# Kernel optimization log

Measured on AMD Instinct MI355X. Metric: run time of the kernel, lower is better.

## Reference

```python
import jax, jax.numpy as jnp
import numpy as np

B, H, W = 4, 240, 1216
PROP = 6


def conv2d(x, w, b, pad=0, groups=1):
    out = jax.lax.conv_general_dilated(
        x, w, (1, 1), ((pad, pad), (pad, pad)),
        dimension_numbers=('NCHW', 'OIHW', 'NCHW'),
        feature_group_count=groups)
    return out + b[None, :, None, None]


def affinity(g, ww, wb, ow, ob):
    # g: [B,8,H,W] -> offset [B,18,H,W] (y,x pairs per kernel pt), weight [B,9,H,W]
    wgt = jax.nn.sigmoid(conv2d(g, ww, wb, pad=1))
    wgt = wgt / (jnp.sum(wgt, axis=1, keepdims=True) + 1e-8)
    off = conv2d(g, ow, ob, pad=1)                      # [B,16,H,W]
    off = off.reshape(B, 8, 2, H, W)
    zero = jnp.zeros((B, 1, 2, H, W), off.dtype)
    off = jnp.concatenate([off[:, :4], zero, off[:, 4:]], axis=1)  # zero offset at reference (center) point, idx 4
    return off.reshape(B, 18, H, W), wgt


def bilinear_gather(img, py, px):
    # img [B,H,W]; py/px [B,9,H,W]; zero padding outside the image
    y0 = jnp.floor(py); x0 = jnp.floor(px)
    wy = py - y0; wx = px - x0
    y0i = y0.astype(jnp.int32); x0i = x0.astype(jnp.int32)
    flat = img.reshape(B, -1)
    out = jnp.zeros_like(py)
    for dy, dx, wgt in ((0, 0, (1 - wy) * (1 - wx)), (0, 1, (1 - wy) * wx),
                        (1, 0, wy * (1 - wx)), (1, 1, wy * wx)):
        yy = y0i + dy; xx = x0i + dx
        valid = (yy >= 0) & (yy < H) & (xx >= 0) & (xx < W)
        idx = (jnp.clip(yy, 0, H - 1) * W + jnp.clip(xx, 0, W - 1)).reshape(B, -1)
        v = jnp.take_along_axis(flat, idx, axis=1).reshape(B, 9, H, W)
        out = out + wgt * jnp.where(valid, v, 0.0)
    return out


def mdconv(feat, offset, mask, w3, b3):
    # Modulated deformable conv (DCNv2), 3x3, stride 1, pad 1, dil 1,
    # groups = C = 1, weight w3 [1,1,3,3] (ones), bias b3 [1] (zero).
    off = offset.reshape(B, 9, 2, H, W)
    ky = jnp.repeat(jnp.arange(3), 3).astype(feat.dtype)   # kernel row for k = i*3+j
    kx = jnp.tile(jnp.arange(3), 3).astype(feat.dtype)
    gy = jnp.arange(H, dtype=feat.dtype)
    gx = jnp.arange(W, dtype=feat.dtype)
    py = gy[None, None, :, None] - 1.0 + ky[None, :, None, None] + off[:, :, 0]
    px = gx[None, None, None, :] - 1.0 + kx[None, :, None, None] + off[:, :, 1]
    samp = bilinear_gather(feat[:, 0], py, px)             # [B,9,H,W]
    out = jnp.einsum('bkhw,k->bhw', mask * samp, w3.reshape(9)) + b3[0]
    return out[:, None]


def _forward(feat_init, guidance, attn, aff_w_w, aff_w_b, aff_o_w, aff_o_b,
             w3, b3, proj_w, bn_g, bn_b, c0_w, c0_b, cs_w, cs_b,
             c1_w, c1_b, c2_w, c2_b, csq_w, csq_b, cv_w, cv_b):
    feats = []
    feat = feat_init
    for k in range(PROP):  # fixed, small structural loop (distinct params per step)
        g = guidance[:, 8 * k:8 * (k + 1)]
        off, wgt = affinity(g, aff_w_w[k], aff_w_b[k], aff_o_w[k], aff_o_b[k])
        feat = mdconv(feat, off, wgt, w3, b3)
        feats.append(feat)
    y = jnp.concatenate(feats[3:6], axis=1)                # [B,3,H,W]
    # proj: 1x1 conv (no bias) -> BatchNorm (training-mode stats) -> LeakyReLU(0.2)
    sf = conv2d(y, proj_w, jnp.zeros((6,), y.dtype), pad=0)
    mu = jnp.mean(sf, axis=(0, 2, 3), keepdims=True)
    var = jnp.var(sf, axis=(0, 2, 3), keepdims=True)
    sf = (sf - mu) * jax.lax.rsqrt(var + 1e-5)
    sf = sf * bn_g[None, :, None, None] + bn_b[None, :, None, None]
    sf = jnp.where(sf > 0, sf, 0.2 * sf)
    x = jnp.concatenate([attn, sf], axis=1)                # [B,22,H,W]
    # CrossAttn(dim=22)
    a1 = conv2d(x, c0_w, c0_b, pad=0, groups=22)           # depthwise 1x1
    a2 = conv2d(a1, cs_w, cs_b, pad=1, groups=22)          # depthwise 3x3
    a1 = conv2d(a1, c1_w, c1_b)                            # 22 -> 11
    a2 = conv2d(a2, c2_w, c2_b)                            # 22 -> 11
    ac = jnp.concatenate([a1, a2], axis=1)                 # [B,22,H,W]
    agg = jnp.concatenate([jnp.mean(ac, axis=1, keepdims=True),
                           jnp.max(ac, axis=1, keepdims=True)], axis=1)
    sig = jax.nn.sigmoid(conv2d(agg, csq_w, csq_b, pad=1))
    a = a1 * sig[:, 0:1] + a2 * sig[:, 1:2]
    a = conv2d(a, cv_w, cv_b)                              # [B,3,H,W]
    return jnp.sum(y * a, axis=1, keepdims=True)           # [B,1,H,W]


def setup_inputs() -> dict:
    key = jax.random.key(0)
    ks = jax.random.split(key, 16)
    n = lambda k, s, sc=1.0: sc * jax.random.normal(k, s, dtype=jnp.float32)
    return {
        'feat_init': n(ks[0], (B, 1, H, W)),
        'guidance': n(ks[1], (B, 48, H, W)),
        'attn': n(ks[2], (B, 16, H, W)),
        'feat_fix': n(ks[3], (B, 1, H, W)),
        'aff_w_w': n(ks[4], (PROP, 9, 8, 3, 3), 0.1),
        'aff_w_b': jnp.zeros((PROP, 9), jnp.float32),
        'aff_o_w': n(ks[5], (PROP, 16, 8, 3, 3), 0.05),
        'aff_o_b': jnp.zeros((PROP, 16), jnp.float32),
        'w3': jnp.ones((1, 1, 3, 3), jnp.float32),
        'b3': jnp.zeros((1,), jnp.float32),
        'proj_w': n(ks[6], (6, 3, 1, 1), 0.3),
        'bn_g': jnp.ones((6,), jnp.float32),
        'bn_b': jnp.zeros((6,), jnp.float32),
        'c0_w': n(ks[7], (22, 1, 1, 1), 0.3),
        'c0_b': jnp.zeros((22,), jnp.float32),
        'cs_w': n(ks[8], (22, 1, 3, 3), 0.2),
        'cs_b': jnp.zeros((22,), jnp.float32),
        'c1_w': n(ks[9], (11, 22, 1, 1), 0.2),
        'c1_b': jnp.zeros((11,), jnp.float32),
        'c2_w': n(ks[10], (11, 22, 1, 1), 0.2),
        'c2_b': jnp.zeros((11,), jnp.float32),
        'csq_w': n(ks[11], (2, 2, 3, 3), 0.2),
        'csq_b': jnp.zeros((2,), jnp.float32),
        'cv_w': n(ks[12], (3, 11, 1, 1), 0.2),
        'cv_b': jnp.zeros((3,), jnp.float32),
    }


def reference(feat_init, guidance, attn, feat_fix, aff_w_w, aff_w_b, aff_o_w, aff_o_b,
              w3, b3, proj_w, bn_g, bn_b, c0_w, c0_b, cs_w, cs_b,
              c1_w, c1_b, c2_w, c2_b, csq_w, csq_b, cv_w, cv_b):
    # mask_fix = sign(feat_fix) is computed in the original but never used.
    _ = jnp.sign(feat_fix)
    return _forward(feat_init, guidance, attn, aff_w_w, aff_w_b, aff_o_w, aff_o_b,
                    w3, b3, proj_w, bn_g, bn_b, c0_w, c0_b, cs_w, cs_b,
                    c1_w, c1_b, c2_w, c2_b, csq_w, csq_b, cv_w, cv_b)
```

## Files before the change

### kernel.cpp

```cpp
#include <hip/hip_runtime.h>
#include <hip/hip_bf16.h>
#include <math.h>

#define HH 240
#define WW 1216
#define BATCH 4
#define PROP 6
constexpr int HW = HH * WW;
constexpr int NPIX = BATCH * HW;
constexpr int NPART = 1024;

typedef short short8 __attribute__((ext_vector_type(8)));
typedef float floatx4 __attribute__((ext_vector_type(4)));

__device__ __forceinline__ unsigned short f2bf(float f) {
    unsigned int u = __float_as_uint(f);
    unsigned int r = (u + 0x7FFFu + ((u >> 16) & 1u)) >> 16;
    return (unsigned short)r;
}
__device__ __forceinline__ float bf2f(unsigned short h) {
    return __uint_as_float(((unsigned int)h) << 16);
}

constexpr int CT_STRIDE = 25;
constexpr int SMEM_BYTES = 23360;

__global__ __launch_bounds__(256, 4) void prop_kernel(
    const float* __restrict__ featPrev,
    const float* __restrict__ gbase,
    const float* __restrict__ aw,
    const float* __restrict__ ab,
    const float* __restrict__ ow,
    const float* __restrict__ ob,
    const float* __restrict__ w3,
    const float* __restrict__ b3,
    float* __restrict__ featNext)
{
    __shared__ __attribute__((aligned(16))) unsigned char smem[SMEM_BYTES];
    unsigned short* gs16 = (unsigned short*)smem;
    float*    wst    = (float*)(smem + 10560);
    uint32_t* offtab = (uint32_t*)(smem + 22848);
    unsigned short* ctb = (unsigned short*)(smem + 10560);

    const int tid = threadIdx.x;
    const int x0 = blockIdx.x * 64;
    const int y0t = blockIdx.y * 8;
    const int b = blockIdx.z;
    const float* gb = gbase + (size_t)b * (48 * HW);
    const float* fb = featPrev + (size_t)b * HW;

    for (int idx = tid; idx < 5280; idx += 256) {
        const int c = idx / 660, rem = idx - c * 660;
        const int row = rem / 66, col = rem - row * 66;
        const int gy = y0t + row - 1, gx = x0 + col - 1;
        float v = 0.0f;
        if (((unsigned)gy < (unsigned)HH) & ((unsigned)gx < (unsigned)WW))
            v = gb[c * HW + gy * WW + gx];
        gs16[idx] = f2bf(v);
    }
    for (int idx = tid; idx < 3072; idx += 256) {
        const int o = idx / 96, k = idx - o * 96;
        float v = 0.0f;
        if (o < 25 && k < 72) {
            const int c = k / 9, t = k - 9 * c;
            v = (o < 9) ? aw[(o * 8 + c) * 9 + t] : ow[((o - 9) * 8 + c) * 9 + t];
        }
        wst[idx] = v;
    }
    if (tid < 96) {
        const int s = tid >> 5, rem = tid & 31, e = rem >> 2, gq = rem & 3;
        const int k = s * 32 + gq * 8 + e;
        uint32_t off = 0;
        if (k < 72) {
            const int c = k / 9, t = k - 9 * c, dy = t / 3, dx = t - 3 * dy;
            off = (uint32_t)(c * 660 + dy * 66 + dx);
        }
        offtab[tid] = off;
    }
    __syncthreads();

    const int lane = tid & 63, wid = tid >> 6;
    const int grp = lane >> 4, l15 = lane & 15;

    short8 Ah0[3], Ah1[3], Al0[3], Al1[3];
    {
        const int kb = grp * 8;
#pragma unroll
        for (int s = 0; s < 3; ++s) {
            const float* wp0 = &wst[l15 * 96 + s * 32 + kb];
            const float* wp1 = &wst[(16 + l15) * 96 + s * 32 + kb];
            short8 h0, l0, h1, l1;
#pragma unroll
            for (int e = 0; e < 8; ++e) {
                const float v0 = wp0[e];
                const unsigned short hb0 = f2bf(v0);
                h0[e] = (short)hb0;
                l0[e] = (short)f2bf(v0 - bf2f(hb0));
                const float v1 = wp1[e];
                const unsigned short hb1 = f2bf(v1);
                h1[e] = (short)hb1;
                l1[e] = (short)f2bf(v1 - bf2f(hb1));
            }
            Ah0[s] = h0; Al0[s] = l0; Ah1[s] = h1; Al1[s] = l1;
        }
    }

    uint32_t cvaddr[3][8];
#pragma unroll
    for (int s = 0; s < 3; ++s)
#pragma unroll
        for (int e = 0; e < 8; ++e)
            cvaddr[s][e] = (offtab[s * 32 + e * 4 + grp] +
                            (uint32_t)(wid * 132 + l15)) * 2u;

    float abv[9], w3v[9], obv[16];
#pragma unroll
    for (int t = 0; t < 9; ++t) { abv[t] = ab[t]; w3v[t] = w3[t]; }
#pragma unroll
    for (int o = 0; o < 16; ++o) obv[o] = ob[o];
    const float b3v = b3[0];

    __syncthreads();

    unsigned short* ct = ctb + wid * (64 * CT_STRIDE);
    const int ybase = y0t + wid * 2;
    const unsigned char* gsB = (const unsigned char*)gs16;

#pragma unroll 1
    for (int r = 0; r < 2; ++r) {
        const int y = ybase + r;
#pragma unroll
        for (int ch = 0; ch < 4; ++ch) {
            floatx4 acc0 = {0.f, 0.f, 0.f, 0.f};
            floatx4 acc1 = {0.f, 0.f, 0.f, 0.f};
#pragma unroll
            for (int s = 0; s < 3; ++s) {
                uint32_t ev[8];
#pragma unroll
                for (int e = 0; e < 8; ++e)
                    ev[e] = *(const unsigned short*)(gsB + cvaddr[s][e] +
                                                     (r * 66 + ch * 16) * 2);
                union { uint32_t u[4]; short8 v; } bh;
#pragma unroll
                for (int i = 0; i < 4; ++i)
                    bh.u[i] = ev[2 * i] | (ev[2 * i + 1] << 16);
                acc0 = __builtin_amdgcn_mfma_f32_16x16x32_bf16(Ah0[s], bh.v, acc0, 0, 0, 0);
                acc1 = __builtin_amdgcn_mfma_f32_16x16x32_bf16(Ah1[s], bh.v, acc1, 0, 0, 0);
                acc0 = __builtin_amdgcn_mfma_f32_16x16x32_bf16(Al0[s], bh.v, acc0, 0, 0, 0);
                acc1 = __builtin_amdgcn_mfma_f32_16x16x32_bf16(Al1[s], bh.v, acc1, 0, 0, 0);
            }
            const int pxb = (ch * 16 + l15) * CT_STRIDE;
#pragma unroll
            for (int i = 0; i < 4; ++i) {
                ct[pxb + grp * 4 + i] = f2bf(acc0[i]);
                if (grp * 4 + i < 9)
                    ct[pxb + 16 + grp * 4 + i] = f2bf(acc1[i]);
            }
        }

        const unsigned short* cb = ct + lane * CT_STRIDE;
        float av[25];
#pragma unroll
        for (int o = 0; o < 25; ++o) av[o] = bf2f(cb[o]);

        float wg[9], wsum = 1e-8f;
#pragma unroll
        for (int t = 0; t < 9; ++t) {
            const float s = 1.0f / (1.0f + __expf(-(av[t] + abv[t])));
            wg[t] = s;
            wsum += s;
        }
        const float winv = 1.0f / wsum;
        const int x = x0 + lane;

        float sum = 0.0f;
#pragma unroll
        for (int t = 0; t < 9; ++t) {
            float oy, ox;
            if (t < 4)       { oy = av[9 + 2 * t] + obv[2 * t];
                               ox = av[10 + 2 * t] + obv[2 * t + 1]; }
            else if (t == 4) { oy = 0.0f; ox = 0.0f; }
            else             { oy = av[7 + 2 * t] + obv[2 * t - 2];
                               ox = av[8 + 2 * t] + obv[2 * t - 1]; }

            const float py = (float)(y - 1 + (t / 3)) + oy;
            const float px = (float)(x - 1 + (t % 3)) + ox;
            const float fy = floorf(py), fx = floorf(px);
            const float wy = py - fy, wx = px - fx;
            const int iy = (int)fy, ix = (int)fx;
            const int iy1 = iy + 1, ix1 = ix + 1;

            const int ry0 = min(max(iy, 0), HH - 1) * WW;
            const int ry1 = min(max(iy1, 0), HH - 1) * WW;
            const int cx0 = min(max(ix, 0), WW - 1);
            const int cx1 = min(max(ix1, 0), WW - 1);
            const float v00 = fb[ry0 + cx0], v01 = fb[ry0 + cx1];
            const float v10 = fb[ry1 + cx0], v11 = fb[ry1 + cx1];

            const bool vy0 = (unsigned)iy < (unsigned)HH;
            const bool vy1 = (unsigned)iy1 < (unsigned)HH;
            const bool vx0 = (unsigned)ix < (unsigned)WW;
            const bool vx1 = (unsigned)ix1 < (unsigned)WW;
            const float wy0 = 1.0f - wy, wx0 = 1.0f - wx;

            float s = 0.0f;
            s = fmaf((vy0 & vx0) ? wy0 * wx0 : 0.0f, v00, s);
            s = fmaf((vy0 & vx1) ? wy0 * wx  : 0.0f, v01, s);
            s = fmaf((vy1 & vx0) ? wy  * wx0 : 0.0f, v10, s);
            s = fmaf((vy1 & vx1) ? wy  * wx  : 0.0f, v11, s);

            sum = fmaf(wg[t] * w3v[t], s, sum);
        }
        featNext[(size_t)b * HW + (size_t)y * WW + x] = fmaf(winv, sum, b3v);
    }
}

__global__ __launch_bounds__(256) void stats_part(
    const float* __restrict__ y0s, const float* __restrict__ y1s,
    const float* __restrict__ y2s, float* __restrict__ part)
{
    float a[9] = {0, 0, 0, 0, 0, 0, 0, 0, 0};
    const int n4 = NPIX / 4;
    const int stride = gridDim.x * 256;
    for (int i = blockIdx.x * 256 + threadIdx.x; i < n4; i += stride) {
        const float4 q0 = ((const float4*)y0s)[i];
        const float4 q1 = ((const float4*)y1s)[i];
        const float4 q2 = ((const float4*)y2s)[i];
        const float v0s[4] = {q0.x, q0.y, q0.z, q0.w};
        const float v1s[4] = {q1.x, q1.y, q1.z, q1.w};
        const float v2s[4] = {q2.x, q2.y, q2.z, q2.w};
#pragma unroll
        for (int j = 0; j < 4; ++j) {
            const float v0 = v0s[j], v1 = v1s[j], v2 = v2s[j];
            a[0] += v0; a[1] += v1; a[2] += v2;
            a[3] = fmaf(v0, v0, a[3]); a[4] = fmaf(v0, v1, a[4]);
            a[5] = fmaf(v0, v2, a[5]); a[6] = fmaf(v1, v1, a[6]);
            a[7] = fmaf(v1, v2, a[7]); a[8] = fmaf(v2, v2, a[8]);
        }
    }
    __shared__ float red[4][9];
    const int lane = threadIdx.x & 63, wv = threadIdx.x >> 6;
#pragma unroll
    for (int q = 0; q < 9; ++q) {
        float v = a[q];
        for (int o = 32; o; o >>= 1) v += __shfl_down(v, o, 64);
        if (lane == 0) red[wv][q] = v;
    }
    __syncthreads();
    if (threadIdx.x < 9) {
        const int q = threadIdx.x;
        part[blockIdx.x * 9 + q] = red[0][q] + red[1][q] + red[2][q] + red[3][q];
    }
}

__global__ __launch_bounds__(256) void stats_final(
    const float* __restrict__ part, const float* __restrict__ proj_w,
    const float* __restrict__ bn_g, const float* __restrict__ bn_b,
    float* __restrict__ stats)
{
    float a[9] = {0, 0, 0, 0, 0, 0, 0, 0, 0};
    for (int i = threadIdx.x; i < NPART; i += 256) {
#pragma unroll
        for (int q = 0; q < 9; ++q) a[q] += part[i * 9 + q];
    }
    __shared__ float red[4][9];
    const int lane = threadIdx.x & 63, wv = threadIdx.x >> 6;
#pragma unroll
    for (int q = 0; q < 9; ++q) {
        float v = a[q];
        for (int o = 32; o; o >>= 1) v += __shfl_down(v, o, 64);
        if (lane == 0) red[wv][q] = v;
    }
    __syncthreads();
    if (threadIdx.x == 0) {
        float s[9];
#pragma unroll
        for (int q = 0; q < 9; ++q) s[q] = red[0][q] + red[1][q] + red[2][q] + red[3][q];
        const float invN = 1.0f / (float)NPIX;
        const float m0 = s[0] * invN, m1 = s[1] * invN, m2 = s[2] * invN;
        const float E00 = s[3] * invN, E01 = s[4] * invN, E02 = s[5] * invN;
        const float E11 = s[6] * invN, E12 = s[7] * invN, E22 = s[8] * invN;
#pragma unroll
        for (int c = 0; c < 6; ++c) {
            const float p0 = proj_w[c * 3], p1 = proj_w[c * 3 + 1], p2 = proj_w[c * 3 + 2];
            const float mu = p0 * m0 + p1 * m1 + p2 * m2;
            const float e2 = p0 * p0 * E00 + p1 * p1 * E11 + p2 * p2 * E22 +
                             2.0f * (p0 * p1 * E01 + p0 * p2 * E02 + p1 * p2 * E12);
            const float var = e2 - mu * mu;
            const float sc = bn_g[c] / sqrtf(var + 1e-5f);
            stats[c] = sc;
            stats[6 + c] = bn_b[c] - mu * sc;
        }
    }
}

constexpr int HB_X = WW / 32;
constexpr int HB_Y = HH / 8;
constexpr int HB_N = HB_X * HB_Y * BATCH;
constexpr int HB_CHUNK = HB_N / 8;

__global__ __launch_bounds__(256, 4) void head_kernel(
    const float* __restrict__ y0s, const float* __restrict__ y1s,
    const float* __restrict__ y2s, const float* __restrict__ attn,
    const float* __restrict__ stats,
    const float* __restrict__ proj_w,
    const float* __restrict__ c0_w, const float* __restrict__ c0_b,
    const float* __restrict__ cs_w, const float* __restrict__ cs_b,
    const float* __restrict__ c1_w, const float* __restrict__ c1_b,
    const float* __restrict__ c2_w, const float* __restrict__ c2_b,
    const float* __restrict__ csq_w, const float* __restrict__ csq_b,
    const float* __restrict__ cv_w, const float* __restrict__ cv_b,
    float* __restrict__ out)
{
    __shared__ float ap[22][432];
    __shared__ float aggs[2][340];

    const int tid = threadIdx.x;
    const int bid = blockIdx.x;
    const int swz = (bid & 7) * HB_CHUNK + (bid >> 3);
    const int b = swz / (HB_X * HB_Y);
    const int rem0 = swz - b * (HB_X * HB_Y);
    const int by = rem0 / HB_X;
    const int bx = rem0 - by * HB_X;
    const int x0 = bx * 32;
    const int y0t = by * 8;

    for (int job = tid; job < 2040; job += 256) {
        int c = 0, rr, xc;
        bool isY;
        if (job < 1920) {
            c = job / 120;
            const int rem = job - c * 120;
            rr = rem / 10; xc = rem - rr * 10;
            isY = false;
        } else {
            const int rem = job - 1920;
            rr = rem / 10; xc = rem - rr * 10;
            isY = true;
        }
        const int gy = y0t + rr - 2;
        const int gxb = x0 - 4 + 4 * xc;
        const bool gok = ((unsigned)gy < (unsigned)HH) &
                         ((unsigned)gxb <= (unsigned)(WW - 4));
        const size_t prow = (size_t)gy * WW + gxb;

        if (!isY) {
            float4 v4 = {0.f, 0.f, 0.f, 0.f};
            if (gok)
                v4 = *(const float4*)&attn[(size_t)b * 16 * HW + (size_t)c * HW + prow];
            const float w = c0_w[c], bb = c0_b[c];
            const float vin[4] = {v4.x, v4.y, v4.z, v4.w};
#pragma unroll
            for (int j = 0; j < 4; ++j) {
                const int exl = 4 * xc - 2 + j;
                if ((unsigned)exl < 36u)
                    ap[c][rr * 36 + exl] = gok ? fmaf(w, vin[j], bb) : 0.0f;
            }
        } else {
            float4 q0 = {0.f, 0.f, 0.f, 0.f}, q1 = q0, q2 = q0;
            if (gok) {
                const size_t p = (size_t)b * HW + prow;
                q0 = *(const float4*)&y0s[p];
                q1 = *(const float4*)&y1s[p];
                q2 = *(const float4*)&y2s[p];
            }
            const float v0s[4] = {q0.x, q0.y, q0.z, q0.w};
            const float v1s[4] = {q1.x, q1.y, q1.z, q1.w};
            const float v2s[4] = {q2.x, q2.y, q2.z, q2.w};
#pragma unroll
            for (int j = 0; j < 4; ++j) {
                const int exl = 4 * xc - 2 + j;
                if ((unsigned)exl >= 36u) continue;
#pragma unroll
                for (int q = 0; q < 6; ++q) {
                    float v = 0.0f;
                    if (gok) {
                        const float sraw = proj_w[q * 3] * v0s[j] +
                                           proj_w[q * 3 + 1] * v1s[j] +
                                           proj_w[q * 3 + 2] * v2s[j];
                        float sf = fmaf(stats[q], sraw, stats[6 + q]);
                        sf = sf > 0.0f ? sf : 0.2f * sf;
                        v = fmaf(c0_w[16 + q], sf, c0_b[16 + q]);
                    }
                    ap[16 + q][rr * 36 + exl] = v;
                }
            }
        }
    }
    __syncthreads();

    auto compute_px = [&](int ay, int ax, float* a1, float* a2) {
        const int ey = ay + 1, ex = ax + 1;
#pragma unroll
        for (int j = 0; j < 11; ++j) { a1[j] = c1_b[j]; a2[j] = c2_b[j]; }
#pragma unroll
        for (int c = 0; c < 22; ++c) {
            float dw = cs_b[c];
            float ctr = 0.0f;
#pragma unroll
            for (int t = 0; t < 9; ++t) {
                const float av = ap[c][(ey + t / 3 - 1) * 36 + (ex + t % 3 - 1)];
                dw = fmaf(cs_w[c * 9 + t], av, dw);
                if (t == 4) ctr = av;
            }
#pragma unroll
            for (int j = 0; j < 11; ++j) {
                a1[j] = fmaf(c1_w[j * 22 + c], ctr, a1[j]);
                a2[j] = fmaf(c2_w[j * 22 + c], dw, a2[j]);
            }
        }
    };

    if (tid < 84) {
        int ay, ax;
        if (tid < 34)      { ay = 0; ax = tid; }
        else if (tid < 68) { ay = 9; ax = tid - 34; }
        else { const int s = tid - 68; ay = 1 + (s >> 1); ax = (s & 1) ? 33 : 0; }
        const int gy = y0t + ay - 1, gx = x0 + ax - 1;
        float m0 = 0.0f, m1 = 0.0f;
        if (((unsigned)gy < (unsigned)HH) & ((unsigned)gx < (unsigned)WW)) {
            float a1h[11], a2h[11];
            compute_px(ay, ax, a1h, a2h);
            float s = 0.0f, mx = -INFINITY;
#pragma unroll
            for (int j = 0; j < 11; ++j) {
                s += a1h[j] + a2h[j];
                mx = fmaxf(mx, fmaxf(a1h[j], a2h[j]));
            }
            m0 = s * (1.0f / 22.0f);
            m1 = mx;
        }
        aggs[0][ay * 34 + ax] = m0;
        aggs[1][ay * 34 + ax] = m1;
    }

    const int ty = tid >> 5, tx = tid & 31;
    const int ay = ty + 1, ax = tx + 1;
    float a1[11], a2[11];
    compute_px(ay, ax, a1, a2);
    {
        float s = 0.0f, mx = -INFINITY;
#pragma unroll
        for (int j = 0; j < 11; ++j) {
            s += a1[j] + a2[j];
            mx = fmaxf(mx, fmaxf(a1[j], a2[j]));
        }
        aggs[0][ay * 34 + ax] = s * (1.0f / 22.0f);
        aggs[1][ay * 34 + ax] = mx;
    }
    __syncthreads();

    float z0 = csq_b[0], z1 = csq_b[1];
#pragma unroll
    for (int t = 0; t < 9; ++t) {
        const int ai = (ay + t / 3 - 1) * 34 + (ax + t % 3 - 1);
        const float g0 = aggs[0][ai], g1 = aggs[1][ai];
        z0 = fmaf(csq_w[t], g0, fmaf(csq_w[9 + t], g1, z0));
        z1 = fmaf(csq_w[18 + t], g0, fmaf(csq_w[27 + t], g1, z1));
    }
    const float s0 = 1.0f / (1.0f + __expf(-z0));
    const float s1 = 1.0f / (1.0f + __expf(-z1));
    float v0 = cv_b[0], v1 = cv_b[1], v2 = cv_b[2];
#pragma unroll
    for (int j = 0; j < 11; ++j) {
        const float av = a1[j] * s0 + a2[j] * s1;
        v0 = fmaf(cv_w[j], av, v0);
        v1 = fmaf(cv_w[11 + j], av, v1);
        v2 = fmaf(cv_w[22 + j], av, v2);
    }
    const size_t p = (size_t)b * HW + (size_t)(y0t + ty) * WW + (x0 + tx);
    out[p] = y0s[p] * v0 + y1s[p] * v1 + y2s[p] * v2;
}

extern "C" void kernel_launch(void* const* d_in, const int* in_sizes, int n_in,
                              void* d_out, int out_size, void* d_ws, size_t ws_size,
                              hipStream_t stream)
{
    (void)in_sizes; (void)n_in; (void)out_size; (void)ws_size;
    const float* feat_init = (const float*)d_in[0];
    const float* guidance  = (const float*)d_in[1];
    const float* attn      = (const float*)d_in[2];
    const float* aff_w_w   = (const float*)d_in[4];
    const float* aff_w_b   = (const float*)d_in[5];
    const float* aff_o_w   = (const float*)d_in[6];
    const float* aff_o_b   = (const float*)d_in[7];
    const float* w3        = (const float*)d_in[8];
    const float* b3        = (const float*)d_in[9];
    const float* proj_w    = (const float*)d_in[10];
    const float* bn_g      = (const float*)d_in[11];
    const float* bn_b      = (const float*)d_in[12];
    const float* c0_w      = (const float*)d_in[13];
    const float* c0_b      = (const float*)d_in[14];
    const float* cs_w      = (const float*)d_in[15];
    const float* cs_b      = (const float*)d_in[16];
    const float* c1_w      = (const float*)d_in[17];
    const float* c1_b      = (const float*)d_in[18];
    const float* c2_w      = (const float*)d_in[19];
    const float* c2_b      = (const float*)d_in[20];
    const float* csq_w     = (const float*)d_in[21];
    const float* csq_b     = (const float*)d_in[22];
    const float* cv_w      = (const float*)d_in[23];
    const float* cv_b      = (const float*)d_in[24];

    float* ws = (float*)d_ws;
    float* slot[5];
    for (int i = 0; i < 5; ++i) slot[i] = ws + (size_t)i * NPIX;
    float* part  = ws + (size_t)5 * NPIX;
    float* stats = part + (size_t)9 * NPART;

    const dim3 blk(256);
    const dim3 gp(WW / 64, HH / 8, BATCH);

    const int dst_ids[PROP] = {0, 1, 0, 2, 3, 4};
    const float* src = feat_init;
    for (int k = 0; k < PROP; ++k) {
        float* dst = slot[dst_ids[k]];
        prop_kernel<<<gp, blk, 0, stream>>>(
            src, guidance + (size_t)8 * k * HW,
            aff_w_w + (size_t)k * 648, aff_w_b + (size_t)k * 9,
            aff_o_w + (size_t)k * 1152, aff_o_b + (size_t)k * 16,
            w3, b3, dst);
        src = dst;
    }

    stats_part<<<dim3(NPART), blk, 0, stream>>>(slot[2], slot[3], slot[4], part);
    stats_final<<<dim3(1), blk, 0, stream>>>(part, proj_w, bn_g, bn_b, stats);

    head_kernel<<<dim3(HB_N), blk, 0, stream>>>(
        slot[2], slot[3], slot[4], attn, stats, proj_w,
        c0_w, c0_b, cs_w, cs_b, c1_w, c1_b, c2_w, c2_b,
        csq_w, csq_b, cv_w, cv_b, (float*)d_out);
}
```

Measured before the change: 628.8 us.

## Split propagation into one batched affinity conv kernel and per-step gather kernels

The affinity convolutions for all six propagation steps depend only on guidance, not on the propagated feature. This change computes them up front in a single launch covering PROP*BATCH slices and writes the 25 bf16 affinity channels per pixel to a global workspace. Each step then runs a lightweight gather kernel that reads those channels and does the deformable bilinear sampling. The batched launch gives more parallel work, but the cost is a large extra global write and read of bf16 intermediates instead of keeping them in LDS.

```diff
diff --git a/kernel.cpp b/kernel.cpp
--- a/kernel.cpp
+++ b/kernel.cpp
@@ -22,32 +22,28 @@
     return __uint_as_float(((unsigned int)h) << 16);
 }
 
-constexpr int CT_STRIDE = 25;
-constexpr int SMEM_BYTES = 23360;
-
-__global__ __launch_bounds__(256, 4) void prop_kernel(
-    const float* __restrict__ featPrev,
-    const float* __restrict__ gbase,
-    const float* __restrict__ aw,
-    const float* __restrict__ ab,
-    const float* __restrict__ ow,
-    const float* __restrict__ ob,
-    const float* __restrict__ w3,
-    const float* __restrict__ b3,
-    float* __restrict__ featNext)
+constexpr int A_SMEM = 23232;
+
+__global__ __launch_bounds__(256, 4) void affinity_kernel(
+    const float* __restrict__ guidance,
+    const float* __restrict__ aff_w_w,
+    const float* __restrict__ aff_o_w,
+    unsigned short* __restrict__ ctg)
 {
-    __shared__ __attribute__((aligned(16))) unsigned char smem[SMEM_BYTES];
+    __shared__ __attribute__((aligned(16))) unsigned char smem[A_SMEM];
     unsigned short* gs16 = (unsigned short*)smem;
     float*    wst    = (float*)(smem + 10560);
     uint32_t* offtab = (uint32_t*)(smem + 22848);
-    unsigned short* ctb = (unsigned short*)(smem + 10560);
 
     const int tid = threadIdx.x;
     const int x0 = blockIdx.x * 64;
     const int y0t = blockIdx.y * 8;
-    const int b = blockIdx.z;
-    const float* gb = gbase + (size_t)b * (48 * HW);
-    const float* fb = featPrev + (size_t)b * HW;
+    const int k = blockIdx.z >> 2;
+    const int b = blockIdx.z & 3;
+    const float* gb = guidance + (size_t)b * (48 * HW) + (size_t)8 * k * HW;
+    const float* aw = aff_w_w + (size_t)k * 648;
+    const float* ow = aff_o_w + (size_t)k * 1152;
+    unsigned short* cg = ctg + (size_t)k * 25 * BATCH * HW + (size_t)b * HW;
 
     for (int idx = tid; idx < 5280; idx += 256) {
         const int c = idx / 660, rem = idx - c * 660;
@@ -59,20 +55,20 @@
         gs16[idx] = f2bf(v);
     }
     for (int idx = tid; idx < 3072; idx += 256) {
-        const int o = idx / 96, k = idx - o * 96;
+        const int o = idx / 96, kk = idx - o * 96;
         float v = 0.0f;
-        if (o < 25 && k < 72) {
-            const int c = k / 9, t = k - 9 * c;
+        if (o < 25 && kk < 72) {
+            const int c = kk / 9, t = kk - 9 * c;
             v = (o < 9) ? aw[(o * 8 + c) * 9 + t] : ow[((o - 9) * 8 + c) * 9 + t];
         }
         wst[idx] = v;
     }
     if (tid < 96) {
         const int s = tid >> 5, rem = tid & 31, e = rem >> 2, gq = rem & 3;
-        const int k = s * 32 + gq * 8 + e;
+        const int kk = s * 32 + gq * 8 + e;
         uint32_t off = 0;
-        if (k < 72) {
-            const int c = k / 9, t = k - 9 * c, dy = t / 3, dx = t - 3 * dy;
+        if (kk < 72) {
+            const int c = kk / 9, t = kk - 9 * c, dy = t / 3, dx = t - 3 * dy;
             off = (uint32_t)(c * 660 + dy * 66 + dx);
         }
         offtab[tid] = off;
@@ -113,16 +109,6 @@
             cvaddr[s][e] = (offtab[s * 32 + e * 4 + grp] +
                             (uint32_t)(wid * 132 + l15)) * 2u;
 
-    float abv[9], w3v[9], obv[16];
-#pragma unroll
-    for (int t = 0; t < 9; ++t) { abv[t] = ab[t]; w3v[t] = w3[t]; }
-#pragma unroll
-    for (int o = 0; o < 16; ++o) obv[o] = ob[o];
-    const float b3v = b3[0];
-
-    __syncthreads();
-
-    unsigned short* ct = ctb + wid * (64 * CT_STRIDE);
     const int ybase = y0t + wid * 2;
     const unsigned char* gsB = (const unsigned char*)gs16;
 
@@ -149,70 +135,94 @@
                 acc0 = __builtin_amdgcn_mfma_f32_16x16x32_bf16(Al0[s], bh.v, acc0, 0, 0, 0);
                 acc1 = __builtin_amdgcn_mfma_f32_16x16x32_bf16(Al1[s], bh.v, acc1, 0, 0, 0);
             }
-            const int pxb = (ch * 16 + l15) * CT_STRIDE;
+            const size_t pxg = (size_t)y * WW + x0 + ch * 16 + l15;
 #pragma unroll
             for (int i = 0; i < 4; ++i) {
-                ct[pxb + grp * 4 + i] = f2bf(acc0[i]);
-                if (grp * 4 + i < 9)
-                    ct[pxb + 16 + grp * 4 + i] = f2bf(acc1[i]);
-            }
-        }
-
-        const unsigned short* cb = ct + lane * CT_STRIDE;
-        float av[25];
-#pragma unroll
-        for (int o = 0; o < 25; ++o) av[o] = bf2f(cb[o]);
-
-        float wg[9], wsum = 1e-8f;
-#pragma unroll
-        for (int t = 0; t < 9; ++t) {
-            const float s = 1.0f / (1.0f + __expf(-(av[t] + abv[t])));
-            wg[t] = s;
-            wsum += s;
-        }
-        const float winv = 1.0f / wsum;
-        const int x = x0 + lane;
-
-        float sum = 0.0f;
-#pragma unroll
-        for (int t = 0; t < 9; ++t) {
-            float oy, ox;
-            if (t < 4)       { oy = av[9 + 2 * t] + obv[2 * t];
-                               ox = av[10 + 2 * t] + obv[2 * t + 1]; }
-            else if (t == 4) { oy = 0.0f; ox = 0.0f; }
-            else             { oy = av[7 + 2 * t] + obv[2 * t - 2];
-                               ox = av[8 + 2 * t] + obv[2 * t - 1]; }
-
-            const float py = (float)(y - 1 + (t / 3)) + oy;
-            const float px = (float)(x - 1 + (t % 3)) + ox;
-            const float fy = floorf(py), fx = floorf(px);
-            const float wy = py - fy, wx = px - fx;
-            const int iy = (int)fy, ix = (int)fx;
-            const int iy1 = iy + 1, ix1 = ix + 1;
-
-            const int ry0 = min(max(iy, 0), HH - 1) * WW;
-            const int ry1 = min(max(iy1, 0), HH - 1) * WW;
-            const int cx0 = min(max(ix, 0), WW - 1);
-            const int cx1 = min(max(ix1, 0), WW - 1);
-            const float v00 = fb[ry0 + cx0], v01 = fb[ry0 + cx1];
-            const float v10 = fb[ry1 + cx0], v11 = fb[ry1 + cx1];
-
-            const bool vy0 = (unsigned)iy < (unsigned)HH;
-            const bool vy1 = (unsigned)iy1 < (unsigned)HH;
-            const bool vx0 = (unsigned)ix < (unsigned)WW;
-            const bool vx1 = (unsigned)ix1 < (unsigned)WW;
-            const float wy0 = 1.0f - wy, wx0 = 1.0f - wx;
-
-            float s = 0.0f;
-            s = fmaf((vy0 & vx0) ? wy0 * wx0 : 0.0f, v00, s);
-            s = fmaf((vy0 & vx1) ? wy0 * wx  : 0.0f, v01, s);
-            s = fmaf((vy1 & vx0) ? wy  * wx0 : 0.0f, v10, s);
-            s = fmaf((vy1 & vx1) ? wy  * wx  : 0.0f, v11, s);
-
-            sum = fmaf(wg[t] * w3v[t], s, sum);
-        }
-        featNext[(size_t)b * HW + (size_t)y * WW + x] = fmaf(winv, sum, b3v);
-    }
+                const int o0 = grp * 4 + i;
+                cg[(size_t)o0 * (BATCH * HW) + pxg] = f2bf(acc0[i]);
+                if (o0 < 9)
+                    cg[(size_t)(16 + o0) * (BATCH * HW) + pxg] = f2bf(acc1[i]);
+            }
+        }
+    }
+}
+
+__global__ __launch_bounds__(256, 4) void gather_kernel(
+    const float* __restrict__ featPrev,
+    const unsigned short* __restrict__ cgk,
+    const float* __restrict__ ab,
+    const float* __restrict__ ob,
+    const float* __restrict__ w3,
+    const float* __restrict__ b3,
+    float* __restrict__ featNext)
+{
+    const int x = blockIdx.x * 256 + threadIdx.x;
+    const int y = blockIdx.y;
+    const int b = blockIdx.z;
+    if (x >= WW) return;
+    const size_t p = (size_t)y * WW + x;
+    const float* fb = featPrev + (size_t)b * HW;
+    const unsigned short* cb = cgk + (size_t)b * HW + p;
+
+    float av[25];
+#pragma unroll
+    for (int o = 0; o < 25; ++o)
+        av[o] = bf2f(cb[(size_t)o * (BATCH * HW)]);
+
+    float abv[9], w3v[9], obv[16];
+#pragma unroll
+    for (int t = 0; t < 9; ++t) { abv[t] = ab[t]; w3v[t] = w3[t]; }
+#pragma unroll
+    for (int o = 0; o < 16; ++o) obv[o] = ob[o];
+
+    float wg[9], wsum = 1e-8f;
+#pragma unroll
+    for (int t = 0; t < 9; ++t) {
+        const float s = 1.0f / (1.0f + __expf(-(av[t] + abv[t])));
+        wg[t] = s;
+        wsum += s;
+    }
+    const float winv = 1.0f / wsum;
+
+    float sum = 0.0f;
+#pragma unroll
+    for (int t = 0; t < 9; ++t) {
+        float oy, ox;
+        if (t < 4)       { oy = av[9 + 2 * t] + obv[2 * t];
+                           ox = av[10 + 2 * t] + obv[2 * t + 1]; }
+        else if (t == 4) { oy = 0.0f; ox = 0.0f; }
+        else             { oy = av[7 + 2 * t] + obv[2 * t - 2];
+                           ox = av[8 + 2 * t] + obv[2 * t - 1]; }
+
+        const float py = (float)(y - 1 + (t / 3)) + oy;
+        const float px = (float)(x - 1 + (t % 3)) + ox;
+        const float fy = floorf(py), fx = floorf(px);
+        const float wy = py - fy, wx = px - fx;
+        const int iy = (int)fy, ix = (int)fx;
+        const int iy1 = iy + 1, ix1 = ix + 1;
+
+        const int ry0 = min(max(iy, 0), HH - 1) * WW;
+        const int ry1 = min(max(iy1, 0), HH - 1) * WW;
+        const int cx0 = min(max(ix, 0), WW - 1);
+        const int cx1 = min(max(ix1, 0), WW - 1);
+        const float v00 = fb[ry0 + cx0], v01 = fb[ry0 + cx1];
+        const float v10 = fb[ry1 + cx0], v11 = fb[ry1 + cx1];
+
+        const bool vy0 = (unsigned)iy < (unsigned)HH;
+        const bool vy1 = (unsigned)iy1 < (unsigned)HH;
+        const bool vx0 = (unsigned)ix < (unsigned)WW;
+        const bool vx1 = (unsigned)ix1 < (unsigned)WW;
+        const float wy0 = 1.0f - wy, wx0 = 1.0f - wx;
+
+        float s = 0.0f;
+        s = fmaf((vy0 & vx0) ? wy0 * wx0 : 0.0f, v00, s);
+        s = fmaf((vy0 & vx1) ? wy0 * wx  : 0.0f, v01, s);
+        s = fmaf((vy1 & vx0) ? wy  * wx0 : 0.0f, v10, s);
+        s = fmaf((vy1 & vx1) ? wy  * wx  : 0.0f, v11, s);
+
+        sum = fmaf(wg[t] * w3v[t], s, sum);
+    }
+    featNext[(size_t)b * HW + p] = fmaf(winv, sum, b3[0]);
 }
 
 __global__ __launch_bounds__(256) void stats_part(
@@ -507,18 +517,20 @@
     for (int i = 0; i < 5; ++i) slot[i] = ws + (size_t)i * NPIX;
     float* part  = ws + (size_t)5 * NPIX;
     float* stats = part + (size_t)9 * NPART;
+    unsigned short* ctg = (unsigned short*)(stats + 16);
 
     const dim3 blk(256);
-    const dim3 gp(WW / 64, HH / 8, BATCH);
+
+    affinity_kernel<<<dim3(WW / 64, HH / 8, PROP * BATCH), blk, 0, stream>>>(
+        guidance, aff_w_w, aff_o_w, ctg);
 
     const int dst_ids[PROP] = {0, 1, 0, 2, 3, 4};
     const float* src = feat_init;
     for (int k = 0; k < PROP; ++k) {
         float* dst = slot[dst_ids[k]];
-        prop_kernel<<<gp, blk, 0, stream>>>(
-            src, guidance + (size_t)8 * k * HW,
-            aff_w_w + (size_t)k * 648, aff_w_b + (size_t)k * 9,
-            aff_o_w + (size_t)k * 1152, aff_o_b + (size_t)k * 16,
+        gather_kernel<<<dim3((WW + 255) / 256, HH, BATCH), blk, 0, stream>>>(
+            src, ctg + (size_t)k * 25 * BATCH * HW,
+            aff_w_b + (size_t)k * 9, aff_o_b + (size_t)k * 16,
             w3, b3, dst);
         src = dst;
     }
```

After: 770.8 us. +22.6%, slower.
